# Performance work log

Measured on AMD Instinct MI355X. Metric: run time of the kernel, lower is better.

## Reference

```python
import jax, jax.numpy as jnp
import numpy as np

STATE_DIM = 4
MEAS_DIM = 2
N_ADAPT = 10
HID = 128
DT = 0.1
Q0_VAR = 0.1 ** 2   # PROCESS_NOISE_STD**2
R_VAR = 0.5 ** 2    # MEAS_NOise_STD**2

F_MAT = jnp.array([[1, 0, DT, 0], [0, 1, 0, DT], [0, 0, 1, 0], [0, 0, 0, 1]], dtype=jnp.float32)
H_MAT = jnp.array([[1, 0, 0, 0], [0, 1, 0, 0]], dtype=jnp.float32)
Q0 = jnp.eye(STATE_DIM, dtype=jnp.float32) * Q0_VAR
R = jnp.eye(MEAS_DIM, dtype=jnp.float32) * R_VAR
I4 = jnp.eye(STATE_DIM, dtype=jnp.float32)


def setup_inputs() -> dict:
    key = jax.random.key(0)
    ks = jax.random.split(key, 8)
    B, T = 1024, 512
    s = 0.1
    return {
        "measurements": jax.random.normal(ks[0], (B, T, MEAS_DIM), jnp.float32),
        "Q_tilde": jnp.eye(STATE_DIM)[None].repeat(N_ADAPT, 0) * 0.001
                   + jax.random.normal(ks[1], (N_ADAPT, STATE_DIM, STATE_DIM), jnp.float32) * 0.001,
        "W_ih": jax.random.normal(ks[2], (4 * HID, MEAS_DIM), jnp.float32) * s,
        "W_hh": jax.random.normal(ks[3], (4 * HID, HID), jnp.float32) * s,
        "b_ih": jax.random.normal(ks[4], (4 * HID,), jnp.float32) * s,
        "b_hh": jax.random.normal(ks[5], (4 * HID,), jnp.float32) * s,
        "W_fc": jax.random.normal(ks[6], (N_ADAPT, HID), jnp.float32) * s,
        "b_fc": jax.random.normal(ks[7], (N_ADAPT,), jnp.float32) * s,
    }


def _nnakf(measurements, Q_tilde, W_ih, W_hh, b_ih, b_hh, W_fc, b_fc):
    B = measurements.shape[0]
    x0 = jnp.zeros((B, STATE_DIM), jnp.float32)
    P0 = jnp.broadcast_to(I4, (B, STATE_DIM, STATE_DIM))
    h0 = jnp.zeros((B, HID), jnp.float32)
    c0 = jnp.zeros((B, HID), jnp.float32)

    def step(carry, z):
        x, P, h, c = carry
        # predict
        x_pred = x @ F_MAT.T                                   # [B,4]
        P_pred0 = jnp.einsum('ij,bjk,lk->bil', F_MAT, P, F_MAT) + Q0
        innov = z - x_pred @ H_MAT.T                           # [B,2]
        S0 = jnp.einsum('ij,bjk,lk->bil', H_MAT, P_pred0, H_MAT) + R
        In = innov ** 2 / jnp.diagonal(S0, axis1=-2, axis2=-1)  # [B,2]
        # LSTM cell (torch gate order i,f,g,o)
        gates = In @ W_ih.T + b_ih + h @ W_hh.T + b_hh          # [B,4H]
        i_g, f_g, g_g, o_g = jnp.split(gates, 4, axis=-1)
        c = jax.nn.sigmoid(f_g) * c + jax.nn.sigmoid(i_g) * jnp.tanh(g_g)
        h = jax.nn.sigmoid(o_g) * jnp.tanh(c)
        sigma = jax.nn.sigmoid(h @ W_fc.T + b_fc)               # [B,N]
        Q_adapt = Q0 + jnp.einsum('bn,nij->bij', sigma, Q_tilde)
        P_pred = P_pred0 - Q0 + Q_adapt
        # update
        S = jnp.einsum('ij,bjk,lk->bil', H_MAT, P_pred, H_MAT) + R   # [B,2,2]
        PHt = jnp.einsum('bij,kj->bik', P_pred, H_MAT)               # [B,4,2]
        K = PHt @ jnp.linalg.inv(S)                                  # [B,4,2]
        x = x_pred + jnp.einsum('bij,bj->bi', K, innov)
        P = (I4 - K @ H_MAT) @ P_pred
        return (x, P, h, c), x

    zs = jnp.swapaxes(measurements, 0, 1)  # [T,B,2]
    _, xs = jax.lax.scan(step, (x0, P0, h0, c0), zs)
    return jnp.swapaxes(xs, 0, 1)          # [B,T,4]


def reference(measurements, Q_tilde, W_ih, W_hh, b_ih, b_hh, W_fc, b_fc):
    return _nnakf(measurements, Q_tilde, W_ih, W_hh, b_ih, b_hh, W_fc, b_fc)
```

## Files before the change

### kernel.cpp

```cpp
#include <hip/hip_runtime.h>
#include <stdint.h>


#define DTc  0.1f
#define Q0V  0.01f
#define RV   0.25f

typedef __bf16 bf16x8 __attribute__((ext_vector_type(8)));
typedef float  f32x4  __attribute__((ext_vector_type(4)));

__device__ __forceinline__ unsigned short f2bf(float f) {
    union { float f; unsigned int ui; } c; c.f = f;
    unsigned int u = c.ui;
    return (unsigned short)((u + 0x7FFFu + ((u >> 16) & 1u)) >> 16);
}
__device__ __forceinline__ bf16x8 cvt8(float4 a, float4 b) {
    union { unsigned short us[8]; bf16x8 v; } r;
    r.us[0] = f2bf(a.x); r.us[1] = f2bf(a.y); r.us[2] = f2bf(a.z); r.us[3] = f2bf(a.w);
    r.us[4] = f2bf(b.x); r.us[5] = f2bf(b.y); r.us[6] = f2bf(b.z); r.us[7] = f2bf(b.w);
    return r.v;
}
__device__ __forceinline__ float rcpf(float x)  { return __builtin_amdgcn_rcpf(x); }
__device__ __forceinline__ float sigmf(float x) { return rcpf(1.0f + __expf(-x)); }
__device__ __forceinline__ float tanhf_(float x){ return 1.0f - 2.0f * rcpf(__expf(2.0f * x) + 1.0f); }

#define QP_ROT2  0x4E
#define QP_BC0   0x00
#define QP_BC1   0x55
template<int CTRL>
__device__ __forceinline__ float dppf(float x) {
    return __builtin_bit_cast(float,
        __builtin_amdgcn_update_dpp(0, __builtin_bit_cast(int, x), CTRL, 0xF, 0xF, true));
}

__global__ __launch_bounds__(256, 1) void nnakf_kernel(
    const float* __restrict__ meas,
    const float* __restrict__ Qt,
    const float* __restrict__ Wih,
    const float* __restrict__ Whh,
    const float* __restrict__ bih,
    const float* __restrict__ bhh,
    const float* __restrict__ Wfc,
    const float* __restrict__ bfc,
    float* __restrict__ out)
{
    __shared__ float          meas_s[4 * 1024];
    __shared__ unsigned short hbuf[2 * 640];
    __shared__ float          sig_s[4 * 64];

    const int tid  = threadIdx.x;
    const int w    = tid >> 6;
    const int lane = tid & 63;
    const int idx  = lane & 15;
    const int q    = lane >> 4;
    const int j    = lane & 3;
    const int bg0  = blockIdx.x * 4;

    {
        const float4* g4 = (const float4*)(meas + (size_t)bg0 * 1024);
        float4* ms4 = (float4*)meas_s;
        for (int k = tid; k < 1024; k += 256) ms4[k] = g4[k];
    }

    bf16x8 wf[8][4];
    float  breg[8];
    const float4* whh4 = (const float4*)Whh;
    #pragma unroll
    for (int t8 = 0; t8 < 8; ++t8) {
        const int nb = ((t8 >> 1) << 7) + (w << 5) + ((t8 & 1) << 4);
        const int n  = nb + idx;
        breg[t8] = bih[n] + bhh[n];
        #pragma unroll
        for (int s = 0; s < 4; ++s) {
            float4 u0 = whh4[n * 32 + s * 8 + q * 2];
            float4 u1 = whh4[n * 32 + s * 8 + q * 2 + 1];
            wf[t8][s] = cvt8(u0, u1);
        }
    }
    bf16x8 fcf[4];
    #pragma unroll
    for (int s = 0; s < 4; ++s) {
        float4 u0 = make_float4(0.f, 0.f, 0.f, 0.f), u1 = u0;
        if (idx < 10) {
            u0 = ((const float4*)Wfc)[idx * 32 + s * 8 + q * 2];
            u1 = ((const float4*)Wfc)[idx * 32 + s * 8 + q * 2 + 1];
        }
        fcf[s] = cvt8(u0, u1);
    }
    const float bfc_r = (idx < 10) ? bfc[idx] : 0.0f;

    float2 wihr[2][4];
    #pragma unroll
    for (int u = 0; u < 2; ++u)
        #pragma unroll
        for (int g = 0; g < 4; ++g)
            wihr[u][g] = ((const float2*)Wih)[g * 128 + w * 32 + u * 16 + idx];

    float qreg[10][4];
    #pragma unroll
    for (int n = 0; n < 10; ++n)
        #pragma unroll
        for (int r = 0; r < 4; ++r) qreg[n][r] = Qt[n * 16 + r * 4 + j];

    float P0 = (j == 0) ? 1.f : 0.f, P1 = (j == 1) ? 1.f : 0.f;
    float P2 = (j == 2) ? 1.f : 0.f, P3 = (j == 3) ? 1.f : 0.f;
    float x0 = 0.f, x1 = 0.f, x2 = 0.f, x3 = 0.f;
    float cst0 = 0.f, cst1 = 0.f;
    float ppc0, ppc1, ppc2, ppc3, xp0, xp1, inn0, inn1, In0, In1;

    f32x4 acc[8];
    #pragma unroll
    for (int t8 = 0; t8 < 8; ++t8)
        acc[t8] = (f32x4){breg[t8], breg[t8], breg[t8], breg[t8]};

    __syncthreads();

    #define PREDICT(TT)                                                          \
    {                                                                            \
        const float fp0 = P0 + DTc * P2, fp1 = P1 + DTc * P3;                    \
        const float d0 = dppf<QP_ROT2>(P0), d1 = dppf<QP_ROT2>(P1);              \
        const float d2 = dppf<QP_ROT2>(P2), d3 = dppf<QP_ROT2>(P3);              \
        const float fq0 = d0 + DTc * d2, fq1 = d1 + DTc * d3;                    \
        const bool jl2 = (j < 2);                                                \
        ppc0 = fp0 + (jl2 ? DTc * fq0 : 0.f) + ((j == 0) ? Q0V : 0.f);           \
        ppc1 = fp1 + (jl2 ? DTc * fq1 : 0.f) + ((j == 1) ? Q0V : 0.f);           \
        ppc2 = P2  + (jl2 ? DTc * d2  : 0.f) + ((j == 2) ? Q0V : 0.f);           \
        ppc3 = P3  + (jl2 ? DTc * d3  : 0.f) + ((j == 3) ? Q0V : 0.f);           \
        xp0 = x0 + DTc * x2; xp1 = x1 + DTc * x3;                                \
        const float2 zz = *(const float2*)&meas_s[q * 1024 + 2 * (TT)];          \
        inn0 = zz.x - xp0; inn1 = zz.y - xp1;                                    \
        const float s000 = dppf<QP_BC0>(ppc0) + RV;                              \
        const float s011 = dppf<QP_BC1>(ppc1) + RV;                              \
        In0 = inn0 * inn0 * rcpf(s000);                                          \
        In1 = inn1 * inn1 * rcpf(s011);                                          \
    }
    PREDICT(0)

    for (int t = 0; t < 512; ++t) {
        unsigned short* hw = &hbuf[(t & 1) * 640];
        #pragma unroll
        for (int u = 0; u < 2; ++u) {
            float pre[4];
            #pragma unroll
            for (int g = 0; g < 4; ++g)
                pre[g] = acc[2 * g + u][0] + In0 * wihr[u][g].x + In1 * wihr[u][g].y;
            const float cprev = u ? cst1 : cst0;
            const float cn = sigmf(pre[1]) * cprev + sigmf(pre[0]) * tanhf_(pre[2]);
            const float hn = sigmf(pre[3]) * tanhf_(cn);
            if (u) cst1 = cn; else cst0 = cn;
            hw[q * 160 + w * 32 + u * 16 + idx] = f2bf(hn);
        }
        __syncthreads();

        bf16x8 af[4];
        #pragma unroll
        for (int s = 0; s < 4; ++s)
            af[s] = __builtin_bit_cast(bf16x8,
                        *(const uint4*)&hw[(idx >> 2) * 160 + s * 32 + q * 8]);

        f32x4 f0 = (f32x4){0.f, 0.f, 0.f, 0.f};
        f32x4 f1 = (f32x4){0.f, 0.f, 0.f, 0.f};
        f0 = __builtin_amdgcn_mfma_f32_16x16x32_bf16(af[0], fcf[0], f0, 0, 0, 0);
        f1 = __builtin_amdgcn_mfma_f32_16x16x32_bf16(af[1], fcf[1], f1, 0, 0, 0);
        f0 = __builtin_amdgcn_mfma_f32_16x16x32_bf16(af[2], fcf[2], f0, 0, 0, 0);
        f1 = __builtin_amdgcn_mfma_f32_16x16x32_bf16(af[3], fcf[3], f1, 0, 0, 0);
        const f32x4 facc = f0 + f1;
        const float sg = sigmf(facc[0] + bfc_r);
        if (idx < 10) sig_s[w * 64 + q * 16 + idx] = sg;

        #pragma unroll
        for (int t8 = 0; t8 < 8; ++t8)
            acc[t8] = (f32x4){breg[t8], breg[t8], breg[t8], breg[t8]};
        #pragma unroll
        for (int s = 0; s < 4; ++s)
            #pragma unroll
            for (int t8 = 0; t8 < 8; ++t8)
                acc[t8] = __builtin_amdgcn_mfma_f32_16x16x32_bf16(af[s], wf[t8][s], acc[t8], 0, 0, 0);

        float sn[10];
        #pragma unroll
        for (int n = 0; n < 10; ++n) sn[n] = sig_s[w * 64 + q * 16 + n];
        float a0 = 0.f, a1 = 0.f, a2 = 0.f, a3 = 0.f;
        float e0 = 0.f, e1 = 0.f, e2 = 0.f, e3 = 0.f;
        #pragma unroll
        for (int n = 0; n < 5; ++n) {
            a0 += sn[n] * qreg[n][0]; a1 += sn[n] * qreg[n][1];
            a2 += sn[n] * qreg[n][2]; a3 += sn[n] * qreg[n][3];
        }
        #pragma unroll
        for (int n = 5; n < 10; ++n) {
            e0 += sn[n] * qreg[n][0]; e1 += sn[n] * qreg[n][1];
            e2 += sn[n] * qreg[n][2]; e3 += sn[n] * qreg[n][3];
        }
        const float pc0 = ppc0 + a0 + e0;
        const float pc1 = ppc1 + a1 + e1;
        const float pc2 = ppc2 + a2 + e2;
        const float pc3 = ppc3 + a3 + e3;

        const float ph00 = dppf<QP_BC0>(pc0), ph01 = dppf<QP_BC1>(pc0);
        const float ph10 = dppf<QP_BC0>(pc1), ph11 = dppf<QP_BC1>(pc1);
        const float ph20 = dppf<QP_BC0>(pc2), ph21 = dppf<QP_BC1>(pc2);
        const float ph30 = dppf<QP_BC0>(pc3), ph31 = dppf<QP_BC1>(pc3);
        const float s00 = ph00 + RV, s01 = ph01, s10 = ph10, s11 = ph11 + RV;
        const float rdet = rcpf(s00 * s11 - s01 * s10);
        const float K00 = (ph00 * s11 - ph01 * s10) * rdet, K01 = (ph01 * s00 - ph00 * s01) * rdet;
        const float K10 = (ph10 * s11 - ph11 * s10) * rdet, K11 = (ph11 * s00 - ph10 * s01) * rdet;
        const float K20 = (ph20 * s11 - ph21 * s10) * rdet, K21 = (ph21 * s00 - ph20 * s01) * rdet;
        const float K30 = (ph30 * s11 - ph31 * s10) * rdet, K31 = (ph31 * s00 - ph30 * s01) * rdet;
        x0 = xp0 + K00 * inn0 + K01 * inn1;
        x1 = xp1 + K10 * inn0 + K11 * inn1;
        x2 = x2  + K20 * inn0 + K21 * inn1;
        x3 = x3  + K30 * inn0 + K31 * inn1;
        P0 = pc0 - K00 * pc0 - K01 * pc1;
        P1 = pc1 - K10 * pc0 - K11 * pc1;
        P2 = pc2 - K20 * pc0 - K21 * pc1;
        P3 = pc3 - K30 * pc0 - K31 * pc1;

        if (w == 0 && idx == 0) {
            float4* o = (float4*)out;
            o[(size_t)(bg0 + q) * 512 + t] = make_float4(x0, x1, x2, x3);
        }

        const int tn = (t < 511) ? t + 1 : 511;
        PREDICT(tn)
    }
}

extern "C" void kernel_launch(void* const* d_in, const int* in_sizes, int n_in,
                              void* d_out, int out_size, void* d_ws, size_t ws_size,
                              hipStream_t stream) {
    (void)in_sizes; (void)n_in; (void)out_size; (void)d_ws; (void)ws_size;
    nnakf_kernel<<<256, 256, 0, stream>>>(
        (const float*)d_in[0],
        (const float*)d_in[1],
        (const float*)d_in[2],
        (const float*)d_in[3],
        (const float*)d_in[4],
        (const float*)d_in[5],
        (const float*)d_in[6],
        (const float*)d_in[7],
        (float*)d_out);
}
```

Before: 539.0 us.

## Split LSTM hidden units across eight waves instead of four per block

Doubles the block to 512 threads so each wave owns 16 hidden units and 4 gate accumulators instead of 32 units and 8. Each wave's per-step MFMA chain and activation work is halved. The bias is now fed directly as the first MFMA accumulator, and the Kalman update is refactored to apply S^-1 to the innovation and covariance before multiplying by PH^T, which removes explicit gain computation. In exchange, the per-step barrier now spans 8 waves, and the Kalman/FC work is duplicated across more waves.

```diff
diff --git a/kernel.cpp b/kernel.cpp
--- a/kernel.cpp
+++ b/kernel.cpp
@@ -33,7 +33,7 @@
         __builtin_amdgcn_update_dpp(0, __builtin_bit_cast(int, x), CTRL, 0xF, 0xF, true));
 }
 
-__global__ __launch_bounds__(256, 1) void nnakf_kernel(
+__global__ __launch_bounds__(512, 2) void nnakf_kernel(
     const float* __restrict__ meas,
     const float* __restrict__ Qt,
     const float* __restrict__ Wih,
@@ -46,7 +46,7 @@
 {
     __shared__ float          meas_s[4 * 1024];
     __shared__ unsigned short hbuf[2 * 640];
-    __shared__ float          sig_s[4 * 64];
+    __shared__ float          sig_s[8 * 64];
 
     const int tid  = threadIdx.x;
     const int w    = tid >> 6;
@@ -55,26 +55,27 @@
     const int q    = lane >> 4;
     const int j    = lane & 3;
     const int bg0  = blockIdx.x * 4;
+    const int hh   = w * 16 + idx;
 
     {
         const float4* g4 = (const float4*)(meas + (size_t)bg0 * 1024);
         float4* ms4 = (float4*)meas_s;
-        for (int k = tid; k < 1024; k += 256) ms4[k] = g4[k];
-    }
-
-    bf16x8 wf[8][4];
-    float  breg[8];
+        for (int k = tid; k < 1024; k += 512) ms4[k] = g4[k];
+    }
+
+    bf16x8 wf[4][4];
+    f32x4  biasC[4];
     const float4* whh4 = (const float4*)Whh;
     #pragma unroll
-    for (int t8 = 0; t8 < 8; ++t8) {
-        const int nb = ((t8 >> 1) << 7) + (w << 5) + ((t8 & 1) << 4);
-        const int n  = nb + idx;
-        breg[t8] = bih[n] + bhh[n];
+    for (int g = 0; g < 4; ++g) {
+        const int n = (g << 7) + hh;
+        const float bb = bih[n] + bhh[n];
+        biasC[g] = (f32x4){bb, bb, bb, bb};
         #pragma unroll
         for (int s = 0; s < 4; ++s) {
             float4 u0 = whh4[n * 32 + s * 8 + q * 2];
             float4 u1 = whh4[n * 32 + s * 8 + q * 2 + 1];
-            wf[t8][s] = cvt8(u0, u1);
+            wf[g][s] = cvt8(u0, u1);
         }
     }
     bf16x8 fcf[4];
@@ -89,12 +90,10 @@
     }
     const float bfc_r = (idx < 10) ? bfc[idx] : 0.0f;
 
-    float2 wihr[2][4];
-    #pragma unroll
-    for (int u = 0; u < 2; ++u)
-        #pragma unroll
-        for (int g = 0; g < 4; ++g)
-            wihr[u][g] = ((const float2*)Wih)[g * 128 + w * 32 + u * 16 + idx];
+    float2 wihr[4];
+    #pragma unroll
+    for (int g = 0; g < 4; ++g)
+        wihr[g] = ((const float2*)Wih)[g * 128 + hh];
 
     float qreg[10][4];
     #pragma unroll
@@ -105,13 +104,12 @@
     float P0 = (j == 0) ? 1.f : 0.f, P1 = (j == 1) ? 1.f : 0.f;
     float P2 = (j == 2) ? 1.f : 0.f, P3 = (j == 3) ? 1.f : 0.f;
     float x0 = 0.f, x1 = 0.f, x2 = 0.f, x3 = 0.f;
-    float cst0 = 0.f, cst1 = 0.f;
+    float cst = 0.f;
     float ppc0, ppc1, ppc2, ppc3, xp0, xp1, inn0, inn1, In0, In1;
 
-    f32x4 acc[8];
-    #pragma unroll
-    for (int t8 = 0; t8 < 8; ++t8)
-        acc[t8] = (f32x4){breg[t8], breg[t8], breg[t8], breg[t8]};
+    f32x4 acc[4];
+    #pragma unroll
+    for (int g = 0; g < 4; ++g) acc[g] = biasC[g];
 
     __syncthreads();
 
@@ -138,17 +136,15 @@
 
     for (int t = 0; t < 512; ++t) {
         unsigned short* hw = &hbuf[(t & 1) * 640];
-        #pragma unroll
-        for (int u = 0; u < 2; ++u) {
+        {
             float pre[4];
             #pragma unroll
             for (int g = 0; g < 4; ++g)
-                pre[g] = acc[2 * g + u][0] + In0 * wihr[u][g].x + In1 * wihr[u][g].y;
-            const float cprev = u ? cst1 : cst0;
-            const float cn = sigmf(pre[1]) * cprev + sigmf(pre[0]) * tanhf_(pre[2]);
+                pre[g] = acc[g][0] + In0 * wihr[g].x + In1 * wihr[g].y;
+            const float cn = sigmf(pre[1]) * cst + sigmf(pre[0]) * tanhf_(pre[2]);
             const float hn = sigmf(pre[3]) * tanhf_(cn);
-            if (u) cst1 = cn; else cst0 = cn;
-            hw[q * 160 + w * 32 + u * 16 + idx] = f2bf(hn);
+            cst = cn;
+            hw[q * 160 + hh] = f2bf(hn);
         }
         __syncthreads();
 
@@ -169,13 +165,13 @@
         if (idx < 10) sig_s[w * 64 + q * 16 + idx] = sg;
 
         #pragma unroll
-        for (int t8 = 0; t8 < 8; ++t8)
-            acc[t8] = (f32x4){breg[t8], breg[t8], breg[t8], breg[t8]};
-        #pragma unroll
-        for (int s = 0; s < 4; ++s)
+        for (int g = 0; g < 4; ++g)
+            acc[g] = __builtin_amdgcn_mfma_f32_16x16x32_bf16(af[0], wf[g][0], biasC[g], 0, 0, 0);
+        #pragma unroll
+        for (int s = 1; s < 4; ++s)
             #pragma unroll
-            for (int t8 = 0; t8 < 8; ++t8)
-                acc[t8] = __builtin_amdgcn_mfma_f32_16x16x32_bf16(af[s], wf[t8][s], acc[t8], 0, 0, 0);
+            for (int g = 0; g < 4; ++g)
+                acc[g] = __builtin_amdgcn_mfma_f32_16x16x32_bf16(af[s], wf[g][s], acc[g], 0, 0, 0);
 
         float sn[10];
         #pragma unroll
@@ -203,18 +199,18 @@
         const float ph30 = dppf<QP_BC0>(pc3), ph31 = dppf<QP_BC1>(pc3);
         const float s00 = ph00 + RV, s01 = ph01, s10 = ph10, s11 = ph11 + RV;
         const float rdet = rcpf(s00 * s11 - s01 * s10);
-        const float K00 = (ph00 * s11 - ph01 * s10) * rdet, K01 = (ph01 * s00 - ph00 * s01) * rdet;
-        const float K10 = (ph10 * s11 - ph11 * s10) * rdet, K11 = (ph11 * s00 - ph10 * s01) * rdet;
-        const float K20 = (ph20 * s11 - ph21 * s10) * rdet, K21 = (ph21 * s00 - ph20 * s01) * rdet;
-        const float K30 = (ph30 * s11 - ph31 * s10) * rdet, K31 = (ph31 * s00 - ph30 * s01) * rdet;
-        x0 = xp0 + K00 * inn0 + K01 * inn1;
-        x1 = xp1 + K10 * inn0 + K11 * inn1;
-        x2 = x2  + K20 * inn0 + K21 * inn1;
-        x3 = x3  + K30 * inn0 + K31 * inn1;
-        P0 = pc0 - K00 * pc0 - K01 * pc1;
-        P1 = pc1 - K10 * pc0 - K11 * pc1;
-        P2 = pc2 - K20 * pc0 - K21 * pc1;
-        P3 = pc3 - K30 * pc0 - K31 * pc1;
+        const float u0 = rdet * (s11 * inn0 - s01 * inn1);
+        const float u1 = rdet * (s00 * inn1 - s10 * inn0);
+        x0 = xp0 + ph00 * u0 + ph01 * u1;
+        x1 = xp1 + ph10 * u0 + ph11 * u1;
+        x2 = x2  + ph20 * u0 + ph21 * u1;
+        x3 = x3  + ph30 * u0 + ph31 * u1;
+        const float w0 = rdet * (s11 * pc0 - s01 * pc1);
+        const float w1 = rdet * (s00 * pc1 - s10 * pc0);
+        P0 = pc0 - ph00 * w0 - ph01 * w1;
+        P1 = pc1 - ph10 * w0 - ph11 * w1;
+        P2 = pc2 - ph20 * w0 - ph21 * w1;
+        P3 = pc3 - ph30 * w0 - ph31 * w1;
 
         if (w == 0 && idx == 0) {
             float4* o = (float4*)out;
@@ -230,7 +226,7 @@
                               void* d_out, int out_size, void* d_ws, size_t ws_size,
                               hipStream_t stream) {
     (void)in_sizes; (void)n_in; (void)out_size; (void)d_ws; (void)ws_size;
-    nnakf_kernel<<<256, 256, 0, stream>>>(
+    nnakf_kernel<<<256, 512, 0, stream>>>(
         (const float*)d_in[0],
         (const float*)d_in[1],
         (const float*)d_in[2],
```

Result: slower. 594.8 us (+10.3%).
